# Optimization experiments

Hardware: AMD Instinct MI355X
Metric: run time of the kernel (lower is better)

The kernel has to match this reference:

```python
import math
import jax, jax.numpy as jnp
import numpy as np

INPUT_DIM = 512
HIDDEN_DIM = 512
BATCH = 8
SEQ_LEN = 4096


def _xavier(key, shape):
    fan_out, fan_in = shape
    limit = math.sqrt(6.0 / (fan_in + fan_out))
    return jax.random.uniform(key, shape, jnp.float32, -limit, limit)


def setup_inputs() -> dict:
    key = jax.random.key(0)
    kx, kA, kB, kC, kD, kWg = jax.random.split(key, 6)
    return {
        "x": jax.random.normal(kx, (BATCH, SEQ_LEN, INPUT_DIM), jnp.float32),
        "A": jax.random.uniform(kA, (HIDDEN_DIM,), jnp.float32, 0.8, 0.95),
        "B": _xavier(kB, (HIDDEN_DIM, INPUT_DIM)),
        "C": _xavier(kC, (HIDDEN_DIM, HIDDEN_DIM)),
        "D": _xavier(kD, (HIDDEN_DIM, INPUT_DIM)),
        "Wg": _xavier(kWg, (HIDDEN_DIM, INPUT_DIM)),
        "bias_h": jnp.zeros((HIDDEN_DIM,), jnp.float32),
        "bias_y": jnp.zeros((HIDDEN_DIM,), jnp.float32),
    }


def reference(x, A, B, C, D, Wg, bias_h, bias_y):
    # x: (b, t, i). Eval mode: dropout is identity.
    hidden_dim = A.shape[0]
    # Precompute all input-dependent per-step terms as batched GEMMs.
    g = jnp.clip(jax.nn.sigmoid(jnp.einsum('bti,hi->bth', x, Wg)), 0.05, 0.95)
    xB = jnp.einsum('bti,hi->bth', x, B)
    # h_t = h_{t-1} + g_t*(A*h_{t-1} + xB_t + bias_h - h_{t-1})
    #     = (1 - g_t*(1 - A)) * h_{t-1} + g_t*(xB_t + bias_h)
    a_coef = 1.0 - g * (1.0 - A)          # (b, t, h)
    b_coef = g * (xB + bias_h)            # (b, t, h)

    def step(h, ab):
        a_t, b_t = ab
        h = a_t * h + b_t
        return h, h

    h0 = jnp.zeros((x.shape[0], hidden_dim), x.dtype)
    _, hs = jax.lax.scan(step, h0, (jnp.swapaxes(a_coef, 0, 1), jnp.swapaxes(b_coef, 0, 1)))
    hs = jnp.swapaxes(hs, 0, 1)           # (b, t, h)

    scale = 1.0 / math.sqrt(hidden_dim)
    y = (jnp.einsum('bth,oh->bto', hs, C) + jnp.einsum('bti,hi->bth', x, D) + bias_y) * scale
    return y
```

## Files before the change

kernel.cpp:

```cpp
#include <hip/hip_runtime.h>
#include <math.h>

#define MTOT 32768
#define KD 512
#define HD 512
#define NB 8
#define TS 4096
#define NCHUNK 64
#define TCHUNK 64

typedef __attribute__((ext_vector_type(8))) short bf16x8;
typedef __attribute__((ext_vector_type(4))) float f32x4;
typedef __attribute__((ext_vector_type(4))) unsigned short us4;

#define GLD16(gsrc, ldst) __builtin_amdgcn_global_load_lds( \
    (const __attribute__((address_space(1))) void*)(gsrc),   \
    (__attribute__((address_space(3))) void*)(ldst), 16, 0, 0)

__device__ __forceinline__ unsigned short f2bf(float f) {
    unsigned u = __float_as_uint(f);
    return (unsigned short)((u + 0x7FFFu + ((u >> 16) & 1u)) >> 16);
}
__device__ __forceinline__ float bf2f(unsigned short u) {
    return __uint_as_float(((unsigned)u) << 16);
}

__global__ __launch_bounds__(256) void cast_all(
    const float* __restrict__ x, const float* __restrict__ B,
    const float* __restrict__ G, const float* __restrict__ C,
    const float* __restrict__ D,
    unsigned short* __restrict__ x16, unsigned short* __restrict__ w16)
{
    const int blk = blockIdx.x;
    const float* src;
    unsigned short* dst;
    int i;
    if (blk < (MTOT * KD / 1024)) {
        src = x; dst = x16;
        i = blk * 1024 + threadIdx.x * 4;
    } else {
        const int r = blk - (MTOT * KD / 1024);
        const int mat = r >> 8;
        src = (mat == 0) ? B : (mat == 1) ? G : (mat == 2) ? C : D;
        dst = w16 + (size_t)mat * (HD * KD);
        i = (r & 255) * 1024 + threadIdx.x * 4;
    }
    float4 v = *(const float4*)(src + i);
    us4 o; o.x = f2bf(v.x); o.y = f2bf(v.y); o.z = f2bf(v.z); o.w = f2bf(v.w);
    *(us4*)(dst + i) = o;
}

__global__ __launch_bounds__(256, 2) void in_gemm_mfma(
    const short* __restrict__ xb, const short* __restrict__ wmat,
    const float* __restrict__ Avec, const float* __restrict__ bias_h,
    unsigned* __restrict__ ab16, float2* __restrict__ chPS)
{
    __shared__ __align__(16) short Xs[2][128 * 64];
    __shared__ __align__(16) short Ws[2][2][64 * 64];
    const int tid = threadIdx.x;
    const int w = tid >> 6, l = tid & 63;
    const int m0 = blockIdx.x * 128;
    const int n0 = blockIdx.y * 64;
    const int wm = (w & 1) * 64;
    const int wn = (w >> 1) * 32;

    int xsrc[4], xdst[4];
    #pragma unroll
    for (int j = 0; j < 4; ++j) {
        const int s = (w * 4 + j) * 64 + l;
        const int r = s >> 3, g = (s & 7) ^ (r & 7);
        xsrc[j] = (m0 + r) * KD + g * 8;
        xdst[j] = (w * 4 + j) * 64 * 8;
    }
    int wsrc[2], wdst[2];
    #pragma unroll
    for (int j = 0; j < 2; ++j) {
        const int s = (w * 2 + j) * 64 + l;
        const int r = s >> 3, g = (s & 7) ^ (r & 7);
        wsrc[j] = (n0 + r) * KD + g * 8;
        wdst[j] = (w * 2 + j) * 64 * 8;
    }

    f32x4 acc[2][4][2];
    #pragma unroll
    for (int a = 0; a < 2; ++a)
        #pragma unroll
        for (int i = 0; i < 4; ++i)
            #pragma unroll
            for (int j = 0; j < 2; ++j) acc[a][i][j] = (f32x4)0.0f;

    #pragma unroll
    for (int j = 0; j < 4; ++j) GLD16(xb + xsrc[j], &Xs[0][xdst[j]]);
    #pragma unroll
    for (int mat = 0; mat < 2; ++mat)
        #pragma unroll
        for (int j = 0; j < 2; ++j)
            GLD16(wmat + (size_t)mat * (HD * KD) + wsrc[j], &Ws[0][mat][wdst[j]]);
    asm volatile("s_waitcnt vmcnt(0)" ::: "memory");
    __builtin_amdgcn_s_barrier();

    #pragma unroll
    for (int it = 0; it < 8; ++it) {
        const int cur = it & 1;
        const int kk = it * 64;
        if (it < 7) {
            #pragma unroll
            for (int j = 0; j < 4; ++j)
                GLD16(xb + xsrc[j] + kk + 64, &Xs[cur ^ 1][xdst[j]]);
            #pragma unroll
            for (int mat = 0; mat < 2; ++mat)
                #pragma unroll
                for (int j = 0; j < 2; ++j)
                    GLD16(wmat + (size_t)mat * (HD * KD) + wsrc[j] + kk + 64,
                          &Ws[cur ^ 1][mat][wdst[j]]);
        }
        __builtin_amdgcn_s_setprio(1);
        #pragma unroll
        for (int kc = 0; kc < 2; ++kc) {
            const int g = kc * 4 + (l >> 4);
            bf16x8 af[4];
            #pragma unroll
            for (int mt = 0; mt < 4; ++mt) {
                const int r = wm + mt * 16 + (l & 15);
                af[mt] = *(const bf16x8*)(&Xs[cur][r * 64 + ((g ^ (r & 7)) * 8)]);
            }
            #pragma unroll
            for (int mat = 0; mat < 2; ++mat) {
                #pragma unroll
                for (int nt = 0; nt < 2; ++nt) {
                    const int r = wn + nt * 16 + (l & 15);
                    bf16x8 bfv = *(const bf16x8*)(&Ws[cur][mat][r * 64 + ((g ^ (r & 7)) * 8)]);
                    #pragma unroll
                    for (int mt = 0; mt < 4; ++mt)
                        acc[mat][mt][nt] = __builtin_amdgcn_mfma_f32_16x16x32_bf16(
                            af[mt], bfv, acc[mat][mt][nt], 0, 0, 0);
                }
            }
        }
        __builtin_amdgcn_s_setprio(0);
        asm volatile("s_waitcnt vmcnt(0)" ::: "memory");
        __builtin_amdgcn_s_barrier();
    }

    const int q  = l >> 4;
    const int cl = l & 15;
    const int bidx   = m0 >> 12;
    const int c_in_b = ((m0 & (TS - 1)) >> 6) + (w & 1);
    #pragma unroll
    for (int nt = 0; nt < 2; ++nt) {
        const int n = n0 + wn + nt * 16 + cl;
        const float An1 = 1.0f - Avec[n];
        const float bh  = bias_h[n];
        float Pc = 1.0f, Sc = 0.0f;
        #pragma unroll
        for (int mt = 0; mt < 4; ++mt) {
            float Pl = 1.0f, Sl = 0.0f;
            #pragma unroll
            for (int r = 0; r < 4; ++r) {
                const float vB = acc[0][mt][nt][r];
                const float vG = acc[1][mt][nt][r];
                float g = __builtin_amdgcn_rcpf(1.0f + __expf(-vG));
                g = fminf(fmaxf(g, 0.05f), 0.95f);
                const unsigned short su = f2bf(g * An1);
                const unsigned short bu = f2bf(g * (vB + bh));
                const float a  = 1.0f - bf2f(su);
                const float bb = bf2f(bu);
                const int m = m0 + wm + mt * 16 + q * 4 + r;
                ab16[(size_t)m * HD + n] = (unsigned)su | ((unsigned)bu << 16);
                Sl = fmaf(a, Sl, bb);
                Pl *= a;
            }
            float Pm = 1.0f, Sm = 0.0f;
            #pragma unroll
            for (int k = 0; k < 4; ++k) {
                const float Pk = __shfl(Pl, cl + 16 * k, 64);
                const float Sk = __shfl(Sl, cl + 16 * k, 64);
                Sm = fmaf(Pk, Sm, Sk);
                Pm *= Pk;
            }
            Sc = fmaf(Pm, Sc, Sm);
            Pc *= Pm;
        }
        if (q == 0) {
            chPS[(size_t)c_in_b * (NB * HD) + bidx * HD + n] = make_float2(Pc, Sc);
        }
    }
}

__global__ __launch_bounds__(256) void scan_pass3(
    const unsigned* __restrict__ ab, const float2* __restrict__ chPS,
    unsigned short* __restrict__ hs_out)
{
    const int g = blockIdx.x * blockDim.x + threadIdx.x;
    const int h = g & (HD - 1);
    const int rest = g >> 9;
    const int b = rest & (NB - 1);
    const int c = rest >> 3;
    const float2* p = chPS + (size_t)b * HD + h;
    float hv = 0.0f;
    for (int j = 0; j < c; ++j) {
        const float2 ps = p[(size_t)j * (NB * HD)];
        hv = fmaf(ps.x, hv, ps.y);
    }
    size_t idx = ((size_t)(b * TS + c * TCHUNK)) * HD + h;
    #pragma unroll 4
    for (int t = 0; t < TCHUNK; ++t) {
        const unsigned v = ab[idx];
        const float a  = 1.0f - bf2f((unsigned short)(v & 0xFFFFu));
        const float bb = bf2f((unsigned short)(v >> 16));
        hv = fmaf(a, hv, bb);
        hs_out[idx] = f2bf(hv);
        idx += HD;
    }
}

__global__ __launch_bounds__(256, 2) void out_gemm_dual(
    const short* __restrict__ hs, const short* __restrict__ xb,
    const short* __restrict__ Cb, const short* __restrict__ Db,
    const float* __restrict__ bias_y, float* __restrict__ y)
{
    __shared__ __align__(16) short As[2][128 * 64];
    __shared__ __align__(16) short Ws[2][128 * 64];
    const int tid = threadIdx.x;
    const int w = tid >> 6, l = tid & 63;
    const int m0 = blockIdx.x * 128;
    const int n0 = blockIdx.y * 128;
    const int wm = (w & 1) * 64;
    const int wn = (w >> 1) * 64;

    int aoff[4], woff[4], dst_s[4];
    #pragma unroll
    for (int j = 0; j < 4; ++j) {
        const int s = (w * 4 + j) * 64 + l;
        const int r = s >> 3, g = (s & 7) ^ (r & 7);
        aoff[j] = (m0 + r) * HD + g * 8;
        woff[j] = (n0 + r) * HD + g * 8;
        dst_s[j] = (w * 4 + j) * 64 * 8;
    }

#define STAGE_OUT(TI, BUF) do {                                         \
    const short* abase_ = (((TI) < 8) ? hs : xb) + ((TI) & 7) * 64;     \
    const short* wbase_ = (((TI) < 8) ? Cb : Db) + ((TI) & 7) * 64;     \
    _Pragma("unroll")                                                   \
    for (int j_ = 0; j_ < 4; ++j_) {                                    \
        GLD16(abase_ + aoff[j_], &As[BUF][dst_s[j_]]);                  \
        GLD16(wbase_ + woff[j_], &Ws[BUF][dst_s[j_]]);                  \
    }                                                                   \
} while (0)

    f32x4 acc[4][4];
    #pragma unroll
    for (int i = 0; i < 4; ++i)
        #pragma unroll
        for (int j = 0; j < 4; ++j) acc[i][j] = (f32x4)0.0f;

    STAGE_OUT(0, 0);
    asm volatile("s_waitcnt vmcnt(0)" ::: "memory");
    __builtin_amdgcn_s_barrier();

    #pragma unroll
    for (int ti = 0; ti < 16; ++ti) {
        const int cur = ti & 1;
        if (ti < 15) STAGE_OUT(ti + 1, cur ^ 1);
        __builtin_amdgcn_s_setprio(1);
        #pragma unroll
        for (int kc = 0; kc < 2; ++kc) {
            const int g = kc * 4 + (l >> 4);
            bf16x8 af[4], bfv[4];
            #pragma unroll
            for (int t = 0; t < 4; ++t) {
                const int ra = wm + t * 16 + (l & 15);
                af[t] = *(const bf16x8*)(&As[cur][ra * 64 + ((g ^ (ra & 7)) * 8)]);
                const int rb = wn + t * 16 + (l & 15);
                bfv[t] = *(const bf16x8*)(&Ws[cur][rb * 64 + ((g ^ (rb & 7)) * 8)]);
            }
            #pragma unroll
            for (int mt = 0; mt < 4; ++mt)
                #pragma unroll
                for (int nt = 0; nt < 4; ++nt)
                    acc[mt][nt] = __builtin_amdgcn_mfma_f32_16x16x32_bf16(
                        af[mt], bfv[nt], acc[mt][nt], 0, 0, 0);
        }
        __builtin_amdgcn_s_setprio(0);
        asm volatile("s_waitcnt vmcnt(0)" ::: "memory");
        __builtin_amdgcn_s_barrier();
    }
#undef STAGE_OUT

    const float scale = 0.04419417382415922f;
    #pragma unroll
    for (int nt = 0; nt < 4; ++nt) {
        const int n = n0 + wn + nt * 16 + (l & 15);
        const float by = bias_y[n];
        #pragma unroll
        for (int mt = 0; mt < 4; ++mt) {
            #pragma unroll
            for (int r = 0; r < 4; ++r) {
                const int m = m0 + wm + mt * 16 + (l >> 4) * 4 + r;
                y[(size_t)m * HD + n] = (acc[mt][nt][r] + by) * scale;
            }
        }
    }
}

extern "C" void kernel_launch(void* const* d_in, const int* in_sizes, int n_in,
                              void* d_out, int out_size, void* d_ws, size_t ws_size,
                              hipStream_t stream) {
    const float* x      = (const float*)d_in[0];
    const float* Avec   = (const float*)d_in[1];
    const float* Bw     = (const float*)d_in[2];
    const float* Cw     = (const float*)d_in[3];
    const float* Dw     = (const float*)d_in[4];
    const float* Wg     = (const float*)d_in[5];
    const float* bias_h = (const float*)d_in[6];
    const float* bias_y = (const float*)d_in[7];
    float* y = (float*)d_out;

    unsigned* ab16        = (unsigned*)d_ws;
    unsigned short* x16   = (unsigned short*)(ab16 + (size_t)MTOT * HD);
    unsigned short* hs16  = x16 + (size_t)MTOT * HD;
    unsigned short* w16   = hs16 + (size_t)MTOT * HD;
    float2* chPS = (float2*)(w16 + (size_t)4 * HD * KD);

    cast_all<<<MTOT * KD / 1024 + 4 * (HD * KD / 1024), 256, 0, stream>>>(
        x, Bw, Wg, Cw, Dw, x16, w16);

    in_gemm_mfma<<<dim3(MTOT / 128, HD / 64), 256, 0, stream>>>(
        (const short*)x16, (const short*)w16, Avec, bias_h, ab16, chPS);

    scan_pass3<<<(NB * HD * NCHUNK) / 256, 256, 0, stream>>>(ab16, chPS, hs16);

    out_gemm_dual<<<dim3(MTOT / 128, HD / 128), 256, 0, stream>>>(
        (const short*)hs16, (const short*)x16,
        (const short*)(w16 + (size_t)2 * HD * KD),
        (const short*)(w16 + (size_t)3 * HD * KD), bias_y, y);
}
```

Baseline: 257.7 us.

## Deepen GEMM prefetch, remap blocks per XCD, vectorize scan over four channels

Both GEMM kernels now issue loads two stages ahead and wait with partial vmcnt counts instead of draining all loads each iteration. They also use a 1D grid with an XCD-aware block mapping, so blocks sharing the same rows of x land on the same XCD for L2 reuse. The scan kernel now handles four hidden channels per thread with 16-byte vector loads and stores, using a quarter as many threads. The risks are subtle wait-count correctness and a scan with less parallelism to hide latency.

New measurement: 249.7 us. 1.03x faster.

```diff
diff --git a/kernel.cpp b/kernel.cpp
--- a/kernel.cpp
+++ b/kernel.cpp
@@ -59,8 +59,11 @@
     __shared__ __align__(16) short Ws[2][2][64 * 64];
     const int tid = threadIdx.x;
     const int w = tid >> 6, l = tid & 63;
-    const int m0 = blockIdx.x * 128;
-    const int n0 = blockIdx.y * 64;
+    const int bid = blockIdx.x;
+    const int xcd = bid & 7;
+    const int jj  = bid >> 3;
+    const int n0  = (jj & 7) * 64;
+    const int m0  = (xcd * 32 + (jj >> 3)) * 128;
     const int wm = (w & 1) * 64;
     const int wn = (w >> 1) * 32;
 
@@ -81,6 +84,19 @@
         wdst[j] = (w * 2 + j) * 64 * 8;
     }
 
+#define STAGE_IN(TI, BUF) do {                                              \
+    const int kk_ = (TI) * 64;                                              \
+    _Pragma("unroll")                                                       \
+    for (int j_ = 0; j_ < 4; ++j_)                                          \
+        GLD16(xb + xsrc[j_] + kk_, &Xs[BUF][xdst[j_]]);                     \
+    _Pragma("unroll")                                                       \
+    for (int m_ = 0; m_ < 2; ++m_)                                          \
+        _Pragma("unroll")                                                   \
+        for (int j_ = 0; j_ < 2; ++j_)                                      \
+            GLD16(wmat + (size_t)m_ * (HD * KD) + wsrc[j_] + kk_,           \
+                  &Ws[BUF][m_][wdst[j_]]);                                  \
+} while (0)
+
     f32x4 acc[2][4][2];
     #pragma unroll
     for (int a = 0; a < 2; ++a)
@@ -89,31 +105,15 @@
             #pragma unroll
             for (int j = 0; j < 2; ++j) acc[a][i][j] = (f32x4)0.0f;
 
-    #pragma unroll
-    for (int j = 0; j < 4; ++j) GLD16(xb + xsrc[j], &Xs[0][xdst[j]]);
-    #pragma unroll
-    for (int mat = 0; mat < 2; ++mat)
-        #pragma unroll
-        for (int j = 0; j < 2; ++j)
-            GLD16(wmat + (size_t)mat * (HD * KD) + wsrc[j], &Ws[0][mat][wdst[j]]);
-    asm volatile("s_waitcnt vmcnt(0)" ::: "memory");
-    __builtin_amdgcn_s_barrier();
+    STAGE_IN(0, 0);
+    STAGE_IN(1, 1);
 
     #pragma unroll
     for (int it = 0; it < 8; ++it) {
         const int cur = it & 1;
-        const int kk = it * 64;
-        if (it < 7) {
-            #pragma unroll
-            for (int j = 0; j < 4; ++j)
-                GLD16(xb + xsrc[j] + kk + 64, &Xs[cur ^ 1][xdst[j]]);
-            #pragma unroll
-            for (int mat = 0; mat < 2; ++mat)
-                #pragma unroll
-                for (int j = 0; j < 2; ++j)
-                    GLD16(wmat + (size_t)mat * (HD * KD) + wsrc[j] + kk + 64,
-                          &Ws[cur ^ 1][mat][wdst[j]]);
-        }
+        if (it < 7) asm volatile("s_waitcnt vmcnt(8)" ::: "memory");
+        else        asm volatile("s_waitcnt vmcnt(0)" ::: "memory");
+        __builtin_amdgcn_s_barrier();
         __builtin_amdgcn_s_setprio(1);
         #pragma unroll
         for (int kc = 0; kc < 2; ++kc) {
@@ -138,9 +138,11 @@
             }
         }
         __builtin_amdgcn_s_setprio(0);
-        asm volatile("s_waitcnt vmcnt(0)" ::: "memory");
+        asm volatile("s_waitcnt lgkmcnt(0)" ::: "memory");
         __builtin_amdgcn_s_barrier();
-    }
+        if (it < 6) STAGE_IN(it + 2, cur);
+    }
+#undef STAGE_IN
 
     const int q  = l >> 4;
     const int cl = l & 15;
@@ -192,24 +194,34 @@
     unsigned short* __restrict__ hs_out)
 {
     const int g = blockIdx.x * blockDim.x + threadIdx.x;
-    const int h = g & (HD - 1);
-    const int rest = g >> 9;
+    const int h4 = (g & 127) * 4;
+    const int rest = g >> 7;
     const int b = rest & (NB - 1);
     const int c = rest >> 3;
-    const float2* p = chPS + (size_t)b * HD + h;
-    float hv = 0.0f;
-    for (int j = 0; j < c; ++j) {
-        const float2 ps = p[(size_t)j * (NB * HD)];
-        hv = fmaf(ps.x, hv, ps.y);
-    }
-    size_t idx = ((size_t)(b * TS + c * TCHUNK)) * HD + h;
+    const float2* p = chPS + (size_t)b * HD + h4;
+    float hv0 = 0.0f, hv1 = 0.0f, hv2 = 0.0f, hv3 = 0.0f;
+    for (int jc = 0; jc < c; ++jc) {
+        const float4 ps01 = *(const float4*)(p + (size_t)jc * (NB * HD));
+        const float4 ps23 = *(const float4*)(p + (size_t)jc * (NB * HD) + 2);
+        hv0 = fmaf(ps01.x, hv0, ps01.y);
+        hv1 = fmaf(ps01.z, hv1, ps01.w);
+        hv2 = fmaf(ps23.x, hv2, ps23.y);
+        hv3 = fmaf(ps23.z, hv3, ps23.w);
+    }
+    size_t idx = ((size_t)(b * TS + c * TCHUNK)) * HD + h4;
     #pragma unroll 4
     for (int t = 0; t < TCHUNK; ++t) {
-        const unsigned v = ab[idx];
-        const float a  = 1.0f - bf2f((unsigned short)(v & 0xFFFFu));
-        const float bb = bf2f((unsigned short)(v >> 16));
-        hv = fmaf(a, hv, bb);
-        hs_out[idx] = f2bf(hv);
+        const uint4 v = *(const uint4*)(ab + idx);
+        const float a0 = 1.0f - bf2f((unsigned short)(v.x & 0xFFFFu));
+        const float a1 = 1.0f - bf2f((unsigned short)(v.y & 0xFFFFu));
+        const float a2 = 1.0f - bf2f((unsigned short)(v.z & 0xFFFFu));
+        const float a3 = 1.0f - bf2f((unsigned short)(v.w & 0xFFFFu));
+        hv0 = fmaf(a0, hv0, bf2f((unsigned short)(v.x >> 16)));
+        hv1 = fmaf(a1, hv1, bf2f((unsigned short)(v.y >> 16)));
+        hv2 = fmaf(a2, hv2, bf2f((unsigned short)(v.z >> 16)));
+        hv3 = fmaf(a3, hv3, bf2f((unsigned short)(v.w >> 16)));
+        us4 o; o.x = f2bf(hv0); o.y = f2bf(hv1); o.z = f2bf(hv2); o.w = f2bf(hv3);
+        *(us4*)(hs_out + idx) = o;
         idx += HD;
     }
 }
@@ -223,8 +235,11 @@
     __shared__ __align__(16) short Ws[2][128 * 64];
     const int tid = threadIdx.x;
     const int w = tid >> 6, l = tid & 63;
-    const int m0 = blockIdx.x * 128;
-    const int n0 = blockIdx.y * 128;
+    const int bid = blockIdx.x;
+    const int xcd = bid & 7;
+    const int jj  = bid >> 3;
+    const int n0  = (jj & 3) * 128;
+    const int m0  = (xcd * 32 + (jj >> 2)) * 128;
     const int wm = (w & 1) * 64;
     const int wn = (w >> 1) * 64;
 
@@ -255,13 +270,14 @@
         for (int j = 0; j < 4; ++j) acc[i][j] = (f32x4)0.0f;
 
     STAGE_OUT(0, 0);
-    asm volatile("s_waitcnt vmcnt(0)" ::: "memory");
-    __builtin_amdgcn_s_barrier();
+    STAGE_OUT(1, 1);
 
     #pragma unroll
     for (int ti = 0; ti < 16; ++ti) {
         const int cur = ti & 1;
-        if (ti < 15) STAGE_OUT(ti + 1, cur ^ 1);
+        if (ti < 15) asm volatile("s_waitcnt vmcnt(8)" ::: "memory");
+        else         asm volatile("s_waitcnt vmcnt(0)" ::: "memory");
+        __builtin_amdgcn_s_barrier();
         __builtin_amdgcn_s_setprio(1);
         #pragma unroll
         for (int kc = 0; kc < 2; ++kc) {
@@ -282,8 +298,9 @@
                         af[mt], bfv[nt], acc[mt][nt], 0, 0, 0);
         }
         __builtin_amdgcn_s_setprio(0);
-        asm volatile("s_waitcnt vmcnt(0)" ::: "memory");
+        asm volatile("s_waitcnt lgkmcnt(0)" ::: "memory");
         __builtin_amdgcn_s_barrier();
+        if (ti < 14) STAGE_OUT(ti + 2, cur);
     }
 #undef STAGE_OUT
 
@@ -325,12 +342,12 @@
     cast_all<<<MTOT * KD / 1024 + 4 * (HD * KD / 1024), 256, 0, stream>>>(
         x, Bw, Wg, Cw, Dw, x16, w16);
 
-    in_gemm_mfma<<<dim3(MTOT / 128, HD / 64), 256, 0, stream>>>(
+    in_gemm_mfma<<<2048, 256, 0, stream>>>(
         (const short*)x16, (const short*)w16, Avec, bias_h, ab16, chPS);
 
-    scan_pass3<<<(NB * HD * NCHUNK) / 256, 256, 0, stream>>>(ab16, chPS, hs16);
-
-    out_gemm_dual<<<dim3(MTOT / 128, HD / 128), 256, 0, stream>>>(
+    scan_pass3<<<(NB * HD * NCHUNK / 4) / 256, 256, 0, stream>>>(ab16, chPS, hs16);
+
+    out_gemm_dual<<<1024, 256, 0, stream>>>(
         (const short*)hs16, (const short*)x16,
         (const short*)(w16 + (size_t)2 * HD * KD),
         (const short*)(w16 + (size_t)3 * HD * KD), bias_y, y);
```
